# Kernel tuning notes

Measured on AMD Instinct MI355X. Metric: run time of the kernel, lower is better.

Reference implementation:

```python
import jax, jax.numpy as jnp
import numpy as np

N_NODES = 100000
N_EDGES = 1000000
IN_DIM = 64
HID = 64
OUT = 64
NEG_SLOPE = 0.2  # PyG GATConv default


def setup_inputs() -> dict:
    key = jax.random.key(0)
    ks = jax.random.split(key, 10)
    x = jax.random.normal(ks[0], (N_NODES, IN_DIM), dtype=jnp.float32)
    edge_index = jax.random.randint(ks[1], (2, N_EDGES), 0, N_NODES, dtype=jnp.int64)
    s = 1.0 / np.sqrt(IN_DIM)
    sh = 1.0 / np.sqrt(HID)
    W_src = jax.random.uniform(ks[2], (IN_DIM, HID), jnp.float32, -s, s)
    W_dst = jax.random.uniform(ks[3], (IN_DIM, HID), jnp.float32, -s, s)
    att_src = jax.random.uniform(ks[4], (HID,), jnp.float32, -sh, sh)
    att_dst = jax.random.uniform(ks[5], (HID,), jnp.float32, -sh, sh)
    bias = jnp.zeros((HID,), jnp.float32)
    W_lin = jax.random.uniform(ks[6], (HID, OUT), jnp.float32, -sh, sh)
    b_lin = jax.random.uniform(ks[7], (OUT,), jnp.float32, -sh, sh)
    return {"x": x, "edge_index": edge_index, "W_src": W_src, "W_dst": W_dst,
            "att_src": att_src, "att_dst": att_dst, "bias": bias,
            "W_lin": W_lin, "b_lin": b_lin}


def reference(x, edge_index, W_src, W_dst, att_src, att_dst, bias, W_lin, b_lin):
    src, tgt = edge_index[0], edge_index[1]
    # Bias-free linear projections (PyG GATConv with tuple in_channels)
    h_src = x @ W_src                      # [N, HID]
    h_dst = x @ W_dst                      # [N, HID]
    a_src = h_src @ att_src                # [N]
    a_dst = h_dst @ att_dst                # [N]
    # Per-edge attention logits: LeakyReLU(a_src[j] + a_dst[i])
    e = a_src[src] + a_dst[tgt]            # [E]
    e = jnp.where(e > 0, e, NEG_SLOPE * e)
    # Segment-softmax over incoming edges of each target node
    seg_max = jax.ops.segment_max(e, tgt, num_segments=N_NODES)  # [N]
    expw = jnp.exp(e - seg_max[tgt])                             # [E]
    denom = jax.ops.segment_sum(expw, tgt, num_segments=N_NODES)  # [N]
    alpha = expw / (denom[tgt] + 1e-16)                          # [E]
    # Scatter-aggregate weighted source features
    msgs = alpha[:, None] * h_src[src]                           # [E, HID]
    out = jax.ops.segment_sum(msgs, tgt, num_segments=N_NODES)   # [N, HID]
    out = out + bias
    # Final linear + ReLU
    return jax.nn.relu(out @ W_lin + b_lin)
```

## Files before the change

### kernel.cpp

```cpp
#include <hip/hip_runtime.h>
#include <hip/hip_fp16.h>
#include <math.h>

#define HID 64
#define CBITS 6
#define CSZ 64
#define MAXB 2048
#define CAP 832
#define CAPH 576
#define PB 896
#define MSB 256

__device__ __forceinline__ float4 f4fma(float a, const float4 b, float4 c) {
    c.x = fmaf(a, b.x, c.x); c.y = fmaf(a, b.y, c.y);
    c.z = fmaf(a, b.z, c.z); c.w = fmaf(a, b.w, c.w);
    return c;
}

__global__ void init_kernel(const float* __restrict__ W_dst,
                            const float* __restrict__ att_dst,
                            float* __restrict__ vdst,
                            int* __restrict__ gcursor, int nbc) {
    if (blockIdx.x == 0 && threadIdx.x < HID) {
        int k = threadIdx.x;
        float acc = 0.0f;
#pragma unroll 8
        for (int h = 0; h < HID; ++h) acc = fmaf(W_dst[k * HID + h], att_dst[h], acc);
        vdst[k] = acc;
    }
    int stride = gridDim.x * blockDim.x;
    for (int i = blockIdx.x * blockDim.x + threadIdx.x; i < nbc; i += stride)
        gcursor[i] = i * CAP;
}

__global__ void __launch_bounds__(256)
mid_kernel(const float* __restrict__ x,
           const float* __restrict__ W_src,
           const float* __restrict__ att_src,
           const float* __restrict__ vdst,
           __half* __restrict__ h_half,
           float* __restrict__ a_src,
           float* __restrict__ a_dst, int N,
           const int* __restrict__ src, const int* __restrict__ tgt,
           int* __restrict__ gcursor, int* __restrict__ rec, int E, int nbc) {
    __shared__ __align__(16) char smraw[25088];
    const int t = threadIdx.x;

    if (blockIdx.x < PB) {
        float4* Ws4  = (float4*)smraw;
        float4* att4 = Ws4 + HID * 16;
        float4* vd4  = att4 + 16;
        float*  xs   = (float*)(vd4 + 16);

        for (int i = t; i < HID * 16; i += 256) Ws4[i] = ((const float4*)W_src)[i];
        if (t < 16) {
            att4[t] = ((const float4*)att_src)[t];
            vd4[t]  = ((const float4*)vdst)[t];
        }

        const int g0 = t >> 4;
        const int s = t & 15;
        const float4* x4 = (const float4*)x;
        uint2* h2 = (uint2*)h_half;
        float4* xs4 = (float4*)xs;

        for (int base = blockIdx.x * 32; base < N; base += PB * 32) {
            __syncthreads();
#pragma unroll
            for (int u = 0; u < 2; ++u) {
                int f = t + u * 256;
                int node = base + (f >> 4);
                xs4[f] = (node < N) ? x4[(long long)node * 16 + (f & 15)]
                                    : make_float4(0, 0, 0, 0);
            }
            __syncthreads();

            const float* xr0 = xs + g0 * HID;
            const float* xr1 = xs + (g0 + 16) * HID;

            float4 acc0 = make_float4(0, 0, 0, 0);
            float4 acc1 = make_float4(0, 0, 0, 0);
#pragma unroll 4
            for (int k = 0; k < HID; ++k) {
                float4 w = Ws4[k * 16 + s];
                acc0 = f4fma(xr0[k], w, acc0);
                acc1 = f4fma(xr1[k], w, acc1);
            }

            float4 av = att4[s], qv = vd4[s];
            float p0 = acc0.x * av.x + acc0.y * av.y + acc0.z * av.z + acc0.w * av.w;
            float p1 = acc1.x * av.x + acc1.y * av.y + acc1.z * av.z + acc1.w * av.w;
            float q0 = xr0[4 * s] * qv.x + xr0[4 * s + 1] * qv.y +
                       xr0[4 * s + 2] * qv.z + xr0[4 * s + 3] * qv.w;
            float q1 = xr1[4 * s] * qv.x + xr1[4 * s + 1] * qv.y +
                       xr1[4 * s + 2] * qv.z + xr1[4 * s + 3] * qv.w;
#pragma unroll
            for (int off = 1; off < 16; off <<= 1) {
                p0 += __shfl_xor(p0, off, 64);
                p1 += __shfl_xor(p1, off, 64);
                q0 += __shfl_xor(q0, off, 64);
                q1 += __shfl_xor(q1, off, 64);
            }

            int n0 = base + g0, n1 = base + g0 + 16;
            if (n0 < N) {
                __half2 lo = __float22half2_rn(make_float2(acc0.x, acc0.y));
                __half2 hi = __float22half2_rn(make_float2(acc0.z, acc0.w));
                uint2 pk; pk.x = *(unsigned*)&lo; pk.y = *(unsigned*)&hi;
                h2[(long long)n0 * 16 + s] = pk;
                if (s == 0) { a_src[n0] = p0; a_dst[n0] = q0; }
            }
            if (n1 < N) {
                __half2 lo = __float22half2_rn(make_float2(acc1.x, acc1.y));
                __half2 hi = __float22half2_rn(make_float2(acc1.z, acc1.w));
                uint2 pk; pk.x = *(unsigned*)&lo; pk.y = *(unsigned*)&hi;
                h2[(long long)n1 * 16 + s] = pk;
                if (s == 0) { a_src[n1] = p1; a_dst[n1] = q1; }
            }
        }
    } else {
        int* lh = (int*)smraw;
        const int bid = blockIdx.x - PB;

        for (int i = t; i < nbc; i += 256) lh[i] = 0;
        __syncthreads();
        int chunk = (E + MSB - 1) / MSB;
        int e0 = bid * chunk;
        int e1 = min(E, e0 + chunk);
        for (int e = e0 + t; e < e1; e += 256)
            atomicAdd(&lh[tgt[e] >> CBITS], 1);
        __syncthreads();
        for (int i = t; i < nbc; i += 256)
            if (lh[i]) lh[i] = atomicAdd(&gcursor[i], lh[i]);
        __syncthreads();
        for (int e = e0 + t; e < e1; e += 256) {
            int s = src[e], tg = tgt[e];
            int bi = tg >> CBITS;
            int pos = atomicAdd(&lh[bi], 1);
            if (pos < (bi + 1) * CAP)
                rec[pos] = (s << CBITS) | (tg & (CSZ - 1));
        }
    }
}

__global__ void __launch_bounds__(256)
sort_gather_kernel(const int* __restrict__ gcursor, const int* __restrict__ rec,
                   const __half* __restrict__ h_half,
                   const float* __restrict__ a_src, const float* __restrict__ a_dst,
                   const float* __restrict__ bias,
                   const float* __restrict__ W_lin, const float* __restrict__ b_lin,
                   float* __restrict__ out, int N) {
    __shared__ float4 Wl4[HID * 16];
    __shared__ float4 bs4[16], bl4[16];
    __shared__ int ssort[CAPH];
    __shared__ int hist[32];
    __shared__ int loff[33];
    __shared__ int cur[32];
    __shared__ int sd[32];

    const int t = threadIdx.x;
    for (int i = t; i < HID * 16; i += 256) Wl4[i] = ((const float4*)W_lin)[i];
    if (t < 16) {
        bs4[t] = ((const float4*)bias)[t];
        bl4[t] = ((const float4*)b_lin)[t];
    }

    const int bk = blockIdx.x >> 1;
    const int half = blockIdx.x & 1;
    const int node0 = (bk << CBITS) + half * 32;
    const int nn = min(32, N - node0);
    const int beg = bk * CAP;
    int cnt = gcursor[bk] - beg;
    if (cnt > CAP) cnt = CAP;

    if (t < 32) hist[t] = 0;
    __syncthreads();
    for (int j = t; j < cnt; j += 256) {
        int tl = rec[beg + j] & (CSZ - 1);
        if ((tl >> 5) == half) atomicAdd(&hist[tl & 31], 1);
    }
    __syncthreads();
    if (t < 32) sd[t] = hist[t];
    __syncthreads();
    for (int off = 1; off < 32; off <<= 1) {
        int v = (t < 32 && t >= off) ? sd[t - off] : 0;
        __syncthreads();
        if (t < 32) sd[t] += v;
        __syncthreads();
    }
    if (t < 32) {
        int e = sd[t] - hist[t];
        loff[t] = e; cur[t] = e;
        if (t == 31) loff[32] = min(sd[31], CAPH);
    }
    __syncthreads();
    for (int j = t; j < cnt; j += 256) {
        int r = rec[beg + j];
        int tl = r & (CSZ - 1);
        if ((tl >> 5) == half) {
            int pos = atomicAdd(&cur[tl & 31], 1);
            if (pos < CAPH) ssort[pos] = r >> CBITS;
        }
    }
    __syncthreads();

    const int lane = t & 63;
    const int w = t >> 6;
    const int g = lane >> 4;
    const int s = lane & 15;
    const int gbase = g << 4;
    const uint2* h2 = (const uint2*)h_half;
    float4* out4 = (float4*)out;

#pragma unroll 1
    for (int r2 = 0; r2 < 2; ++r2) {
        int nloc = w * 8 + r2 * 4 + g;
        int n = node0 + nloc;
        bool act = (nloc < nn);
        float adn = act ? a_dst[n] : 0.0f;
        int jb = min(loff[nloc], CAPH);
        int je = min(loff[nloc + 1], CAPH);

        float4 acc = make_float4(0, 0, 0, 0);
        float dsum = 0.0f;
        int j = jb;
        for (; j + 4 <= je; j += 4) {
            int s0 = ssort[j], s1 = ssort[j + 1], s2 = ssort[j + 2], s3 = ssort[j + 3];
            uint2 r0 = h2[(long long)s0 * 16 + s];
            uint2 r1 = h2[(long long)s1 * 16 + s];
            uint2 r2v = h2[(long long)s2 * 16 + s];
            uint2 r3 = h2[(long long)s3 * 16 + s];
            float v0 = a_src[s0] + adn, v1 = a_src[s1] + adn;
            float v2 = a_src[s2] + adn, v3 = a_src[s3] + adn;
            v0 = (v0 > 0.0f) ? v0 : 0.2f * v0;
            v1 = (v1 > 0.0f) ? v1 : 0.2f * v1;
            v2 = (v2 > 0.0f) ? v2 : 0.2f * v2;
            v3 = (v3 > 0.0f) ? v3 : 0.2f * v3;
            float w0 = __expf(v0), w1 = __expf(v1);
            float w2 = __expf(v2), w3 = __expf(v3);
            dsum += (w0 + w1) + (w2 + w3);
            float2 f0a = __half22float2(*(const __half2*)&r0.x);
            float2 f0b = __half22float2(*(const __half2*)&r0.y);
            float2 f1a = __half22float2(*(const __half2*)&r1.x);
            float2 f1b = __half22float2(*(const __half2*)&r1.y);
            float2 f2a = __half22float2(*(const __half2*)&r2v.x);
            float2 f2b = __half22float2(*(const __half2*)&r2v.y);
            float2 f3a = __half22float2(*(const __half2*)&r3.x);
            float2 f3b = __half22float2(*(const __half2*)&r3.y);
            acc.x = fmaf(w0, f0a.x, fmaf(w1, f1a.x, fmaf(w2, f2a.x, fmaf(w3, f3a.x, acc.x))));
            acc.y = fmaf(w0, f0a.y, fmaf(w1, f1a.y, fmaf(w2, f2a.y, fmaf(w3, f3a.y, acc.y))));
            acc.z = fmaf(w0, f0b.x, fmaf(w1, f1b.x, fmaf(w2, f2b.x, fmaf(w3, f3b.x, acc.z))));
            acc.w = fmaf(w0, f0b.y, fmaf(w1, f1b.y, fmaf(w2, f2b.y, fmaf(w3, f3b.y, acc.w))));
        }
        for (; j < je; ++j) {
            int s0 = ssort[j];
            uint2 r0 = h2[(long long)s0 * 16 + s];
            float v0 = a_src[s0] + adn;
            v0 = (v0 > 0.0f) ? v0 : 0.2f * v0;
            float w0 = __expf(v0);
            dsum += w0;
            float2 f0a = __half22float2(*(const __half2*)&r0.x);
            float2 f0b = __half22float2(*(const __half2*)&r0.y);
            acc.x = fmaf(w0, f0a.x, acc.x);
            acc.y = fmaf(w0, f0a.y, acc.y);
            acc.z = fmaf(w0, f0b.x, acc.z);
            acc.w = fmaf(w0, f0b.y, acc.w);
        }

        float inv = 1.0f / (dsum + 1e-16f);
        float4 bsv = bs4[s];
        float4 r;
        r.x = fmaf(acc.x, inv, bsv.x);
        r.y = fmaf(acc.y, inv, bsv.y);
        r.z = fmaf(acc.z, inv, bsv.z);
        r.w = fmaf(acc.w, inv, bsv.w);

        float4 o = bl4[s];
#pragma unroll 4
        for (int ks = 0; ks < 16; ++ks) {
            float rx = __shfl(r.x, gbase + ks, 64);
            float ry = __shfl(r.y, gbase + ks, 64);
            float rz = __shfl(r.z, gbase + ks, 64);
            float rw = __shfl(r.w, gbase + ks, 64);
            o = f4fma(rx, Wl4[(4 * ks + 0) * 16 + s], o);
            o = f4fma(ry, Wl4[(4 * ks + 1) * 16 + s], o);
            o = f4fma(rz, Wl4[(4 * ks + 2) * 16 + s], o);
            o = f4fma(rw, Wl4[(4 * ks + 3) * 16 + s], o);
        }

        if (act) {
            float4 res;
            res.x = o.x > 0.0f ? o.x : 0.0f;
            res.y = o.y > 0.0f ? o.y : 0.0f;
            res.z = o.z > 0.0f ? o.z : 0.0f;
            res.w = o.w > 0.0f ? o.w : 0.0f;
            out4[(long long)n * 16 + s] = res;
        }
    }
}

extern "C" void kernel_launch(void* const* d_in, const int* in_sizes, int n_in,
                              void* d_out, int out_size, void* d_ws, size_t ws_size,
                              hipStream_t stream) {
    const float* x       = (const float*)d_in[0];
    const int*   edge    = (const int*)d_in[1];
    const float* W_src   = (const float*)d_in[2];
    const float* W_dst   = (const float*)d_in[3];
    const float* att_src = (const float*)d_in[4];
    const float* att_dst = (const float*)d_in[5];
    const float* bias    = (const float*)d_in[6];
    const float* W_lin   = (const float*)d_in[7];
    const float* b_lin   = (const float*)d_in[8];
    float* out = (float*)d_out;

    const int N = in_sizes[0] / HID;
    const int E = in_sizes[1] / 2;
    const int* src = edge;
    const int* tgt = edge + E;
    const int nbc = (N + CSZ - 1) / CSZ;

    __half* h_half  = (__half*)d_ws;
    float*  a_src   = (float*)(h_half + (size_t)N * HID);
    float*  a_dst   = a_src + N;
    float*  vdst    = a_dst + N;
    int*    gcursor = (int*)(vdst + 64);
    int*    rec     = gcursor + MAXB;

    init_kernel<<<8, 256, 0, stream>>>(W_dst, att_dst, vdst, gcursor, nbc);
    mid_kernel<<<PB + MSB, 256, 0, stream>>>(x, W_src, att_src, vdst, h_half,
                                             a_src, a_dst, N,
                                             src, tgt, gcursor, rec, E, nbc);
    sort_gather_kernel<<<nbc * 2, 256, 0, stream>>>(gcursor, rec, h_half, a_src, a_dst,
                                                    bias, W_lin, b_lin, out, N);
}
```

Baseline: 163.4 us.

## Fold W_src into final linear and aggregate raw x instead of projected features

Uses linearity to precompute Wc = W_src·W_lin, vsrc = W_src·att_src, and a combined bias c0 in the init kernel. The mid kernel then only converts x to half precision and computes the two attention scalars, with no per-node 64x64 matmul and no shared-memory weight staging. The gather kernel aggregates half-precision x and applies Wc in its existing epilogue. The projection block count and shared memory are reduced. Rounding moves from h_src to x in fp16, which changes accumulated precision slightly.

```diff
diff --git a/kernel.cpp b/kernel.cpp
--- a/kernel.cpp
+++ b/kernel.cpp
@@ -8,7 +8,7 @@
 #define MAXB 2048
 #define CAP 832
 #define CAPH 576
-#define PB 896
+#define PB 512
 #define MSB 256
 
 __device__ __forceinline__ float4 f4fma(float a, const float4 b, float4 c) {
@@ -17,106 +17,87 @@
     return c;
 }
 
-__global__ void init_kernel(const float* __restrict__ W_dst,
+__global__ void init_kernel(const float* __restrict__ W_src,
+                            const float* __restrict__ W_dst,
+                            const float* __restrict__ att_src,
                             const float* __restrict__ att_dst,
-                            float* __restrict__ vdst,
+                            const float* __restrict__ bias,
+                            const float* __restrict__ W_lin,
+                            const float* __restrict__ b_lin,
+                            float* __restrict__ vsrc, float* __restrict__ vdst,
+                            float* __restrict__ c0, float* __restrict__ Wc,
                             int* __restrict__ gcursor, int nbc) {
-    if (blockIdx.x == 0 && threadIdx.x < HID) {
-        int k = threadIdx.x;
-        float acc = 0.0f;
+    const int t = threadIdx.x;
+    if (blockIdx.x == 0) {
+        int k = t >> 2, jb = (t & 3) * 16;
+#pragma unroll 4
+        for (int j = jb; j < jb + 16; ++j) {
+            float acc = 0.0f;
 #pragma unroll 8
-        for (int h = 0; h < HID; ++h) acc = fmaf(W_dst[k * HID + h], att_dst[h], acc);
-        vdst[k] = acc;
+            for (int h = 0; h < HID; ++h) acc = fmaf(W_src[k * HID + h], W_lin[h * HID + j], acc);
+            Wc[k * HID + j] = acc;
+        }
+        if (t < HID) {
+            float as = 0.0f, ad = 0.0f;
+#pragma unroll 8
+            for (int h = 0; h < HID; ++h) {
+                as = fmaf(W_src[t * HID + h], att_src[h], as);
+                ad = fmaf(W_dst[t * HID + h], att_dst[h], ad);
+            }
+            vsrc[t] = as; vdst[t] = ad;
+        } else if (t < 2 * HID) {
+            int j = t - HID;
+            float acc = b_lin[j];
+#pragma unroll 8
+            for (int h = 0; h < HID; ++h) acc = fmaf(bias[h], W_lin[h * HID + j], acc);
+            c0[j] = acc;
+        }
     }
     int stride = gridDim.x * blockDim.x;
-    for (int i = blockIdx.x * blockDim.x + threadIdx.x; i < nbc; i += stride)
+    for (int i = blockIdx.x * blockDim.x + t; i < nbc; i += stride)
         gcursor[i] = i * CAP;
 }
 
 __global__ void __launch_bounds__(256)
 mid_kernel(const float* __restrict__ x,
-           const float* __restrict__ W_src,
-           const float* __restrict__ att_src,
-           const float* __restrict__ vdst,
-           __half* __restrict__ h_half,
-           float* __restrict__ a_src,
-           float* __restrict__ a_dst, int N,
+           const float* __restrict__ vsrc, const float* __restrict__ vdst,
+           __half* __restrict__ xh,
+           float* __restrict__ a_src, float* __restrict__ a_dst, int N,
            const int* __restrict__ src, const int* __restrict__ tgt,
            int* __restrict__ gcursor, int* __restrict__ rec, int E, int nbc) {
-    __shared__ __align__(16) char smraw[25088];
+    __shared__ __align__(16) char smraw[8192];
     const int t = threadIdx.x;
 
     if (blockIdx.x < PB) {
-        float4* Ws4  = (float4*)smraw;
-        float4* att4 = Ws4 + HID * 16;
-        float4* vd4  = att4 + 16;
-        float*  xs   = (float*)(vd4 + 16);
-
-        for (int i = t; i < HID * 16; i += 256) Ws4[i] = ((const float4*)W_src)[i];
+        float4* vs4 = (float4*)smraw;
+        float4* vd4 = vs4 + 16;
         if (t < 16) {
-            att4[t] = ((const float4*)att_src)[t];
-            vd4[t]  = ((const float4*)vdst)[t];
-        }
-
-        const int g0 = t >> 4;
+            vs4[t] = ((const float4*)vsrc)[t];
+            vd4[t] = ((const float4*)vdst)[t];
+        }
+        __syncthreads();
+
         const int s = t & 15;
+        const int gid = (blockIdx.x * 256 + t) >> 4;
+        const int ngr = PB * 16;
         const float4* x4 = (const float4*)x;
-        uint2* h2 = (uint2*)h_half;
-        float4* xs4 = (float4*)xs;
-
-        for (int base = blockIdx.x * 32; base < N; base += PB * 32) {
-            __syncthreads();
-#pragma unroll
-            for (int u = 0; u < 2; ++u) {
-                int f = t + u * 256;
-                int node = base + (f >> 4);
-                xs4[f] = (node < N) ? x4[(long long)node * 16 + (f & 15)]
-                                    : make_float4(0, 0, 0, 0);
-            }
-            __syncthreads();
-
-            const float* xr0 = xs + g0 * HID;
-            const float* xr1 = xs + (g0 + 16) * HID;
-
-            float4 acc0 = make_float4(0, 0, 0, 0);
-            float4 acc1 = make_float4(0, 0, 0, 0);
-#pragma unroll 4
-            for (int k = 0; k < HID; ++k) {
-                float4 w = Ws4[k * 16 + s];
-                acc0 = f4fma(xr0[k], w, acc0);
-                acc1 = f4fma(xr1[k], w, acc1);
-            }
-
-            float4 av = att4[s], qv = vd4[s];
-            float p0 = acc0.x * av.x + acc0.y * av.y + acc0.z * av.z + acc0.w * av.w;
-            float p1 = acc1.x * av.x + acc1.y * av.y + acc1.z * av.z + acc1.w * av.w;
-            float q0 = xr0[4 * s] * qv.x + xr0[4 * s + 1] * qv.y +
-                       xr0[4 * s + 2] * qv.z + xr0[4 * s + 3] * qv.w;
-            float q1 = xr1[4 * s] * qv.x + xr1[4 * s + 1] * qv.y +
-                       xr1[4 * s + 2] * qv.z + xr1[4 * s + 3] * qv.w;
+        uint2* xh2 = (uint2*)xh;
+
+        for (int n = gid; n < N; n += ngr) {
+            float4 xv = x4[n * 16 + s];
+            float4 a = vs4[s], b = vd4[s];
+            float p = xv.x * a.x + xv.y * a.y + xv.z * a.z + xv.w * a.w;
+            float q = xv.x * b.x + xv.y * b.y + xv.z * b.z + xv.w * b.w;
 #pragma unroll
             for (int off = 1; off < 16; off <<= 1) {
-                p0 += __shfl_xor(p0, off, 64);
-                p1 += __shfl_xor(p1, off, 64);
-                q0 += __shfl_xor(q0, off, 64);
-                q1 += __shfl_xor(q1, off, 64);
+                p += __shfl_xor(p, off, 64);
+                q += __shfl_xor(q, off, 64);
             }
-
-            int n0 = base + g0, n1 = base + g0 + 16;
-            if (n0 < N) {
-                __half2 lo = __float22half2_rn(make_float2(acc0.x, acc0.y));
-                __half2 hi = __float22half2_rn(make_float2(acc0.z, acc0.w));
-                uint2 pk; pk.x = *(unsigned*)&lo; pk.y = *(unsigned*)&hi;
-                h2[(long long)n0 * 16 + s] = pk;
-                if (s == 0) { a_src[n0] = p0; a_dst[n0] = q0; }
-            }
-            if (n1 < N) {
-                __half2 lo = __float22half2_rn(make_float2(acc1.x, acc1.y));
-                __half2 hi = __float22half2_rn(make_float2(acc1.z, acc1.w));
-                uint2 pk; pk.x = *(unsigned*)&lo; pk.y = *(unsigned*)&hi;
-                h2[(long long)n1 * 16 + s] = pk;
-                if (s == 0) { a_src[n1] = p1; a_dst[n1] = q1; }
-            }
+            __half2 lo = __float22half2_rn(make_float2(xv.x, xv.y));
+            __half2 hi = __float22half2_rn(make_float2(xv.z, xv.w));
+            uint2 pk; pk.x = *(unsigned*)&lo; pk.y = *(unsigned*)&hi;
+            xh2[n * 16 + s] = pk;
+            if (s == 0) { a_src[n] = p; a_dst[n] = q; }
         }
     } else {
         int* lh = (int*)smraw;
@@ -145,13 +126,12 @@
 
 __global__ void __launch_bounds__(256)
 sort_gather_kernel(const int* __restrict__ gcursor, const int* __restrict__ rec,
-                   const __half* __restrict__ h_half,
+                   const __half* __restrict__ xh,
                    const float* __restrict__ a_src, const float* __restrict__ a_dst,
-                   const float* __restrict__ bias,
-                   const float* __restrict__ W_lin, const float* __restrict__ b_lin,
+                   const float* __restrict__ Wc, const float* __restrict__ c0,
                    float* __restrict__ out, int N) {
-    __shared__ float4 Wl4[HID * 16];
-    __shared__ float4 bs4[16], bl4[16];
+    __shared__ float4 Wc4[HID * 16];
+    __shared__ float4 c04[16];
     __shared__ int ssort[CAPH];
     __shared__ int hist[32];
     __shared__ int loff[33];
@@ -159,11 +139,8 @@
     __shared__ int sd[32];
 
     const int t = threadIdx.x;
-    for (int i = t; i < HID * 16; i += 256) Wl4[i] = ((const float4*)W_lin)[i];
-    if (t < 16) {
-        bs4[t] = ((const float4*)bias)[t];
-        bl4[t] = ((const float4*)b_lin)[t];
-    }
+    for (int i = t; i < HID * 16; i += 256) Wc4[i] = ((const float4*)Wc)[i];
+    if (t < 16) c04[t] = ((const float4*)c0)[t];
 
     const int bk = blockIdx.x >> 1;
     const int half = blockIdx.x & 1;
@@ -209,7 +186,7 @@
     const int g = lane >> 4;
     const int s = lane & 15;
     const int gbase = g << 4;
-    const uint2* h2 = (const uint2*)h_half;
+    const uint2* h2 = (const uint2*)xh;
     float4* out4 = (float4*)out;
 
 #pragma unroll 1
@@ -226,10 +203,10 @@
         int j = jb;
         for (; j + 4 <= je; j += 4) {
             int s0 = ssort[j], s1 = ssort[j + 1], s2 = ssort[j + 2], s3 = ssort[j + 3];
-            uint2 r0 = h2[(long long)s0 * 16 + s];
-            uint2 r1 = h2[(long long)s1 * 16 + s];
-            uint2 r2v = h2[(long long)s2 * 16 + s];
-            uint2 r3 = h2[(long long)s3 * 16 + s];
+            uint2 r0 = h2[s0 * 16 + s];
+            uint2 r1 = h2[s1 * 16 + s];
+            uint2 r2v = h2[s2 * 16 + s];
+            uint2 r3 = h2[s3 * 16 + s];
             float v0 = a_src[s0] + adn, v1 = a_src[s1] + adn;
             float v2 = a_src[s2] + adn, v3 = a_src[s3] + adn;
             v0 = (v0 > 0.0f) ? v0 : 0.2f * v0;
@@ -254,7 +231,7 @@
         }
         for (; j < je; ++j) {
             int s0 = ssort[j];
-            uint2 r0 = h2[(long long)s0 * 16 + s];
+            uint2 r0 = h2[s0 * 16 + s];
             float v0 = a_src[s0] + adn;
             v0 = (v0 > 0.0f) ? v0 : 0.2f * v0;
             float w0 = __expf(v0);
@@ -268,24 +245,23 @@
         }
 
         float inv = 1.0f / (dsum + 1e-16f);
-        float4 bsv = bs4[s];
         float4 r;
-        r.x = fmaf(acc.x, inv, bsv.x);
-        r.y = fmaf(acc.y, inv, bsv.y);
-        r.z = fmaf(acc.z, inv, bsv.z);
-        r.w = fmaf(acc.w, inv, bsv.w);
-
-        float4 o = bl4[s];
+        r.x = acc.x * inv;
+        r.y = acc.y * inv;
+        r.z = acc.z * inv;
+        r.w = acc.w * inv;
+
+        float4 o = c04[s];
 #pragma unroll 4
         for (int ks = 0; ks < 16; ++ks) {
             float rx = __shfl(r.x, gbase + ks, 64);
             float ry = __shfl(r.y, gbase + ks, 64);
             float rz = __shfl(r.z, gbase + ks, 64);
             float rw = __shfl(r.w, gbase + ks, 64);
-            o = f4fma(rx, Wl4[(4 * ks + 0) * 16 + s], o);
-            o = f4fma(ry, Wl4[(4 * ks + 1) * 16 + s], o);
-            o = f4fma(rz, Wl4[(4 * ks + 2) * 16 + s], o);
-            o = f4fma(rw, Wl4[(4 * ks + 3) * 16 + s], o);
+            o = f4fma(rx, Wc4[(4 * ks + 0) * 16 + s], o);
+            o = f4fma(ry, Wc4[(4 * ks + 1) * 16 + s], o);
+            o = f4fma(rz, Wc4[(4 * ks + 2) * 16 + s], o);
+            o = f4fma(rw, Wc4[(4 * ks + 3) * 16 + s], o);
         }
 
         if (act) {
@@ -294,7 +270,7 @@
             res.y = o.y > 0.0f ? o.y : 0.0f;
             res.z = o.z > 0.0f ? o.z : 0.0f;
             res.w = o.w > 0.0f ? o.w : 0.0f;
-            out4[(long long)n * 16 + s] = res;
+            out4[n * 16 + s] = res;
         }
     }
 }
@@ -319,17 +295,21 @@
     const int* tgt = edge + E;
     const int nbc = (N + CSZ - 1) / CSZ;
 
-    __half* h_half  = (__half*)d_ws;
-    float*  a_src   = (float*)(h_half + (size_t)N * HID);
+    __half* xh      = (__half*)d_ws;
+    float*  a_src   = (float*)(xh + (size_t)N * HID);
     float*  a_dst   = a_src + N;
-    float*  vdst    = a_dst + N;
-    int*    gcursor = (int*)(vdst + 64);
+    float*  vsrc    = a_dst + N;
+    float*  vdst    = vsrc + HID;
+    float*  c0      = vdst + HID;
+    float*  Wc      = c0 + HID;
+    int*    gcursor = (int*)(Wc + HID * HID);
     int*    rec     = gcursor + MAXB;
 
-    init_kernel<<<8, 256, 0, stream>>>(W_dst, att_dst, vdst, gcursor, nbc);
-    mid_kernel<<<PB + MSB, 256, 0, stream>>>(x, W_src, att_src, vdst, h_half,
-                                             a_src, a_dst, N,
+    init_kernel<<<8, 256, 0, stream>>>(W_src, W_dst, att_src, att_dst, bias,
+                                       W_lin, b_lin, vsrc, vdst, c0, Wc,
+                                       gcursor, nbc);
+    mid_kernel<<<PB + MSB, 256, 0, stream>>>(x, vsrc, vdst, xh, a_src, a_dst, N,
                                              src, tgt, gcursor, rec, E, nbc);
-    sort_gather_kernel<<<nbc * 2, 256, 0, stream>>>(gcursor, rec, h_half, a_src, a_dst,
-                                                    bias, W_lin, b_lin, out, N);
-}
+    sort_gather_kernel<<<nbc * 2, 256, 0, stream>>>(gcursor, rec, xh, a_src, a_dst,
+                                                    Wc, c0, out, N);
+}
```

New measurement: 198.9 us. 1.22x slower.
